# Kernel optimization log

Measured on AMD Instinct MI355X. Metric: run time of the kernel, lower is better.

Reference implementation:

```python
import jax, jax.numpy as jnp
import numpy as np

BETA = 0.01
EPS = 1e-6

def conv3x3(x, w, b):
    y = jax.lax.conv_general_dilated(x, w, (1, 1), 'SAME',
                                     dimension_numbers=('NCHW', 'OIHW', 'NCHW'))
    return y + b[None, :, None, None]

def variance_depth_flow(gt, patch, max_depth):
    B, C, H, W = gt.shape
    py, px = H // patch, W // patch
    # [B,C,py,px,P,P]
    p = gt.reshape(B, C, py, patch, px, patch).transpose(0, 1, 2, 4, 3, 5)
    p = jnp.where((p > 0.1) & (p < max_depth), p, jnp.zeros_like(p))
    bn = jnp.log(p[..., 0, :] + EPS)   # north border  [B,C,py,px,P]
    bs = jnp.log(p[..., -1, :] + EPS)  # south
    bw = jnp.log(p[..., :, 0] + EPS)   # west
    be = jnp.log(p[..., :, -1] + EPS)  # east
    def sx(b):  # shift patches left along x (axis=3), zero-pad last column
        return jnp.concatenate([b[:, :, :, 1:], jnp.zeros_like(b[:, :, :, :1])], axis=3)
    def sy(b):  # shift patches up along y (axis=2), zero-pad last row
        return jnp.concatenate([b[:, :, 1:], jnp.zeros_like(b[:, :, :1])], axis=2)
    diffs = [be - sx(bw), bs - sy(bn), be - sx(be), bs - sy(bs), bw - sx(bw),
             bn - sy(bn), bs - sx(bs), be - sy(be), bn - sx(bn), bw - sy(bw)]
    d = jnp.stack([x.sum(-1) for x in diffs], axis=-1)  # [B,C,py,px,10]
    d = d[:, 0].transpose(0, 3, 1, 2) / patch            # [B,10,py,px]
    return d

def smooth_l1(pred, target, beta):
    d = pred - target
    ad = jnp.abs(d)
    return jnp.where(ad < beta, 0.5 * d * d / beta, ad - 0.5 * beta)

def setup_inputs() -> dict:
    key = jax.random.key(0)
    ks = jax.random.split(key, 7)
    B, FC, DC, hw, HW = 32, 256, 64, 64, 512
    feat = jax.random.normal(ks[0], (B, FC, hw, hw), dtype=jnp.float32)
    depth = jax.random.normal(ks[1], (B, DC, hw, hw), dtype=jnp.float32)
    gts = jax.random.uniform(ks[2], (B, 1, HW, HW), dtype=jnp.float32)
    W_att = jax.random.normal(ks[3], (DC, FC, 3, 3), dtype=jnp.float32) * 0.02
    b_att = jnp.zeros((DC,), dtype=jnp.float32)
    W_post = jax.random.normal(ks[4], (10, DC, 3, 3), dtype=jnp.float32) * 0.05
    b_post = jnp.zeros((10,), dtype=jnp.float32)
    return {"feat": feat, "depth": depth, "gts": gts,
            "W_att": W_att, "b_att": b_att, "W_post": W_post, "b_post": b_post}

def reference(feat, depth, gts, W_att, b_att, W_post, b_post):
    max_depth = 80.0
    n, c, h, w = depth.shape
    patch = gts.shape[2] // h
    flow_gradient = variance_depth_flow(gts, patch, max_depth)  # [B,10,h,w]
    att = jax.nn.sigmoid(conv3x3(feat, W_att, b_att))           # [B,DC,h,w]
    ds = conv3x3(att * depth, W_post, b_post)                   # [B,10,h,w]
    diff = smooth_l1(ds, flow_gradient, BETA)
    return diff.sum() / (h * w * ds.shape[0] * ds.shape[1])
```

## Files before the change

kernel.cpp:

```cpp
#include <hip/hip_runtime.h>
#include <hip/hip_bf16.h>


typedef __attribute__((ext_vector_type(4))) float f32x4;
typedef __attribute__((ext_vector_type(8))) short s16x8;
typedef __attribute__((ext_vector_type(4))) unsigned int u32x4;

#define DEVFN __device__ __forceinline__

DEVFN float bf2f(unsigned short u){
  unsigned int x = ((unsigned int)u) << 16;
  float f; __builtin_memcpy(&f, &x, 4); return f;
}
DEVFN unsigned short f2bf(float f){
  unsigned int x; __builtin_memcpy(&x, &f, 4);
  x += 0x7fffu + ((x >> 16) & 1u);
  return (unsigned short)(x >> 16);
}
DEVFN unsigned cvtpk(float lo, float hi){
  unsigned r;
  asm("v_cvt_pk_bf16_f32 %0, %1, %2" : "=v"(r) : "v"(lo), "v"(hi));
  return r;
}

#define ASYNC16(gp, lp) __builtin_amdgcn_global_load_lds( \
    (const __attribute__((address_space(1))) unsigned int*)(gp), \
    (__attribute__((address_space(3))) unsigned int*)(lp), 16, 0, 0)

__global__ void k_weights(const float* __restrict__ Watt, const float* __restrict__ Wpost,
                          unsigned short* __restrict__ WT1, unsigned short* __restrict__ WT2){
  const int t = blockIdx.x * 256 + threadIdx.x;
  const int n1 = 9 * 64 * 256;
  if (t < n1){
    const int tap = t / (64 * 256);
    const int rem = t % (64 * 256);
    const int oc = rem / 256, ic = rem % 256;
    WT1[t] = f2bf(Watt[(oc * 256 + ic) * 9 + tap]);
  }
  const int n2 = 9 * 16 * 64;
  if (t < n2){
    const int tap = t / (16 * 64);
    const int rem = t % (16 * 64);
    const int od = rem / 64, ic = rem % 64;
    const float v = (od < 10) ? Wpost[(od * 64 + ic) * 9 + tap] : 0.0f;
    WT2[t] = f2bf(v);
  }
}

__global__ void k_borders(const float* __restrict__ gts, float* __restrict__ S,
                          float* __restrict__ out){
  const int bid = blockIdx.x, tid = threadIdx.x;
  if (bid == 0 && tid == 0) *out = 0.0f;
  __shared__ float slab[4096];
  const int rel = bid;
  const float* gp = gts + (size_t)rel * 4096;
#pragma unroll
  for (int it = 0; it < 4; ++it){
    const int id = it * 256 + tid;
    *(f32x4*)&slab[id * 4] = *(const f32x4*)&gp[id * 4];
  }
  __syncthreads();
  const int px = tid & 63, border = tid >> 6;
  float s = 0.0f;
#pragma unroll
  for (int i = 0; i < 8; ++i){
    float v;
    if (border == 0)      v = slab[px * 8 + i];
    else if (border == 1) v = slab[7 * 512 + px * 8 + i];
    else if (border == 2) v = slab[i * 512 + px * 8];
    else                  v = slab[i * 512 + px * 8 + 7];
    v = ((v > 0.1f) && (v < 80.0f)) ? v : 0.0f;
    s += __logf(v + 1e-6f);
  }
  S[((size_t)rel * 64 + px) * 4 + border] = s;
}

__global__ __launch_bounds__(256, 2) void k_gemm1(
    const float* __restrict__ feat,
    const unsigned short* __restrict__ WT1,
    const float* __restrict__ batt,
    const float* __restrict__ depth,
    unsigned short* __restrict__ adT)
{
  __shared__ unsigned short As[4 * 17 * 16 * 8];
  __shared__ unsigned short Bs[576 * 32];
  const int t = threadIdx.x;
  const int l = t & 63, wid = t >> 6;
  const int wm = wid & 1, wo = wid >> 1;
  const int b = blockIdx.x >> 5, ytile = blockIdx.x & 31;
  const int y0 = ytile * 2;
  const int fr = l & 15, g = l >> 4;

  f32x4 acc[4][2];
#pragma unroll
  for (int i = 0; i < 4; ++i)
#pragma unroll
    for (int j = 0; j < 2; ++j)
#pragma unroll
      for (int q = 0; q < 4; ++q) acc[i][j][q] = 0.0f;

  if (t < 64){
    const int yy = t >> 4, u = t & 15;
    u32x4 z = {0, 0, 0, 0};
    *(u32x4*)&As[((yy * 17 + 16) * 16 + u) * 8] = z;
  }

  f32x4 hold[8];
  auto loadRow = [&](int c){
    const int yr = y0 - 1 + wid;
    if (yr >= 0 && yr < 64){
      const float* gp = feat + ((size_t)(b * 256 + c * 32 + g * 8)) * 4096
                             + (size_t)yr * 64 + fr * 4;
#pragma unroll
      for (int e = 0; e < 8; ++e) hold[e] = *(const f32x4*)(gp + (size_t)e * 4096);
    } else {
#pragma unroll
      for (int e = 0; e < 8; ++e) hold[e] = f32x4{0.f, 0.f, 0.f, 0.f};
    }
  };
  auto cvtWriteRow = [&](){
#pragma unroll
    for (int o = 0; o < 4; ++o){
      u32x4 pk;
      pk[0] = cvtpk(hold[0][o], hold[1][o]);
      pk[1] = cvtpk(hold[2][o], hold[3][o]);
      pk[2] = cvtpk(hold[4][o], hold[5][o]);
      pk[3] = cvtpk(hold[6][o], hold[7][o]);
      const int u = 4 * ((g ^ fr) & 3) + ((o ^ (fr >> 1)) & 3);
      *(u32x4*)&As[((wid * 17 + fr) * 16 + u) * 8] = pk;
    }
  };
  auto stageB = [&](int c){
#pragma unroll
    for (int it = 0; it < 9; ++it){
      const int idx = it * 256 + t;
      const int row = idx >> 2;
      const int sg = (idx & 3) ^ ((row >> 1) & 3);
      ASYNC16(WT1 + (size_t)row * 256 + c * 32 + sg * 8, &Bs[(size_t)idx * 8]);
    }
  };
  auto compute = [&](){
    const int slotB = (g ^ ((fr >> 1) & 3)) * 8;
#pragma unroll
    for (int tap = 0; tap < 9; ++tap){
      const int dy = tap / 3 - 1, dx = tap % 3 - 1;
      const int yy = wm + dy + 1;
      const int rowb = yy * 17 * 16;
      s16x8 af[4], bfr[2];
#pragma unroll
      for (int i = 0; i < 4; ++i){
        const int x = i * 16 + fr + dx;
        const bool valid = (x >= 0) && (x < 64);
        const int xq = valid ? (x >> 2) : 16;
        const int u = valid ? (4 * ((g ^ (x >> 2)) & 3) + (((x & 3) ^ (x >> 3)) & 3))
                            : 4 * g;
        af[i] = *(const s16x8*)&As[(rowb + xq * 16 + u) * 8];
      }
#pragma unroll
      for (int j = 0; j < 2; ++j)
        bfr[j] = *(const s16x8*)&Bs[(tap * 64 + wo * 32 + j * 16 + fr) * 32 + slotB];
#pragma unroll
      for (int i = 0; i < 4; ++i)
#pragma unroll
        for (int j = 0; j < 2; ++j)
          acc[i][j] = __builtin_amdgcn_mfma_f32_16x16x32_bf16(af[i], bfr[j], acc[i][j], 0, 0, 0);
    }
  };

  loadRow(0);
  stageB(0);
  cvtWriteRow();
  __syncthreads();

  for (int c = 0; c < 8; ++c){
    if (c < 7) loadRow(c + 1);
    compute();
    __syncthreads();
    if (c < 7){
      cvtWriteRow();
      stageB(c + 1);
    }
    __syncthreads();
  }

  const int y = y0 + wm;
#pragma unroll
  for (int j = 0; j < 2; ++j){
    const int oc = wo * 32 + j * 16 + fr;
    const float bb = batt[oc];
    const float* dpt = depth + ((size_t)(b * 64 + oc)) * 4096 + (size_t)y * 64;
    unsigned short* op = adT + ((size_t)(b * 4096 + y * 64)) * 64 + oc;
#pragma unroll
    for (int i = 0; i < 4; ++i){
      const f32x4 dv4 = *(const f32x4*)&dpt[i * 16 + g * 4];
#pragma unroll
      for (int q = 0; q < 4; ++q){
        const int xo = i * 16 + g * 4 + q;
        const float v = acc[i][j][q] + bb;
        const float att = 1.0f / (1.0f + __expf(-v));
        op[(size_t)xo * 64] = f2bf(att * dv4[q]);
      }
    }
  }
}

DEVFN float sel4(f32x4 v, int i){
  const float ab = (i & 1) ? v[1] : v[0];
  const float cd = (i & 1) ? v[3] : v[2];
  return (i & 2) ? cd : ab;
}

__global__ __launch_bounds__(512, 2) void k_gemm2(
    const unsigned short* __restrict__ adT,
    const unsigned short* __restrict__ WT2,
    const float* __restrict__ bpost,
    const f32x4* __restrict__ S,
    float* __restrict__ out)
{
  __shared__ unsigned short As[2][20480];
  __shared__ unsigned short Bs[9216];
  __shared__ float ps[8];
  const int t = threadIdx.x;
  const int l = t & 63, w = t >> 6;
  const int b = blockIdx.x >> 3, ytile = blockIdx.x & 7;
  const int y0 = ytile * 8;
  const int fr = l & 15, g = l >> 4;

  f32x4 acc[4];
#pragma unroll
  for (int i = 0; i < 4; ++i)
#pragma unroll
    for (int q = 0; q < 4; ++q) acc[i][q] = 0.0f;

  auto stageA = [&](int c, int d){
#pragma unroll
    for (int it2 = 0; it2 < 5; ++it2){
      const int it = it2 * 2 + (t >> 8);
      const int yy = y0 - 1 + it;
      const int xx = (t >> 2) & 63, icg = t & 3;
      unsigned short* lp = &As[d][(it * 64 + xx) * 32 + icg * 8];
      if (yy >= 0 && yy < 64){
        const int sg = icg ^ ((xx >> 1) & 3);
        const unsigned short* gp = adT
            + ((size_t)(b * 4096 + yy * 64 + xx)) * 64 + c * 32 + sg * 8;
        ASYNC16(gp, lp);
      } else {
        s16x8 z = {0,0,0,0,0,0,0,0};
        *(s16x8*)lp = z;
      }
    }
  };
#pragma unroll
  for (int it = 0; it < 3; ++it){
    const int idx = it * 512 + t;
    if (idx < 1152){
      const int row = idx >> 3, p = idx & 7;
      const int sg = p ^ (row & 7);
      ASYNC16(WT2 + (size_t)row * 64 + sg * 8, Bs + (size_t)idx * 8);
    }
  }
  stageA(0, 0);
  __syncthreads();

  for (int c = 0; c < 2; ++c){
    if (c == 0) stageA(1, 1);
    const unsigned short* Ab = As[c];
    const int pB = ((c * 4 + g) ^ (fr & 7)) * 8;
    for (int tap = 0; tap < 9; ++tap){
      const int dy = tap / 3 - 1, dx = tap % 3 - 1;
      s16x8 af[4];
#pragma unroll
      for (int i = 0; i < 4; ++i){
        const int xv = i * 16 + fr + dx;
        const bool valid = (xv >= 0) && (xv < 64);
        const int xw = valid ? xv : 0;
        const int slot = (g ^ ((xw >> 1) & 3)) * 8;
        s16x8 v = *(const s16x8*)&Ab[((w + dy + 1) * 64 + xw) * 32 + slot];
        s16x8 z = {0,0,0,0,0,0,0,0};
        af[i] = valid ? v : z;
      }
      const s16x8 bfr = *(const s16x8*)&Bs[(tap * 16 + fr) * 64 + pB];
#pragma unroll
      for (int i = 0; i < 4; ++i)
        acc[i] = __builtin_amdgcn_mfma_f32_16x16x32_bf16(af[i], bfr, acc[i], 0, 0, 0);
    }
    __syncthreads();
  }

  const unsigned aPack = (3u<<0)|(1u<<2)|(3u<<4)|(1u<<6)|(2u<<8)|(0u<<10)|(1u<<12)|(3u<<14)|(0u<<16)|(2u<<18);
  const unsigned bPack = (2u<<0)|(0u<<2)|(3u<<4)|(1u<<6)|(2u<<8)|(0u<<10)|(1u<<12)|(3u<<14)|(0u<<16)|(2u<<18);
  float lsum = 0.0f;
  const int y = y0 + w;
  if (fr < 10){
    const int od = fr;
    const int ai = (aPack >> (2 * od)) & 3;
    const int bi = (bPack >> (2 * od)) & 3;
    const bool xshift = (od & 1) == 0;
    const float bp = bpost[od];
#pragma unroll
    for (int i = 0; i < 4; ++i){
#pragma unroll
      for (int q = 0; q < 4; ++q){
        const int xo = i * 16 + g * 4 + q;
        const size_t gm = (size_t)b * 4096 + (size_t)y * 64 + xo;
        const f32x4 sa = S[gm];
        const bool nb = xshift ? (xo < 63) : (y < 63);
        const size_t ga = xshift ? (nb ? gm + 1 : gm) : (nb ? gm + 64 : gm);
        const f32x4 sbv = S[ga];
        const float sbf = nb ? sel4(sbv, bi) : 0.0f;
        const float flow = (sel4(sa, ai) - sbf) * 0.125f;
        const float dv = acc[i][q] + bp - flow;
        const float adv = fabsf(dv);
        lsum += (adv < 0.01f) ? (50.0f * dv * dv) : (adv - 0.005f);
      }
    }
  }
#pragma unroll
  for (int off = 32; off > 0; off >>= 1) lsum += __shfl_down(lsum, off);
  if (l == 0) ps[w] = lsum;
  __syncthreads();
  if (t == 0){
    float s = 0.0f;
#pragma unroll
    for (int i = 0; i < 8; ++i) s += ps[i];
    atomicAdd(out, s * (1.0f / 1310720.0f));
  }
}

extern "C" void kernel_launch(void* const* d_in, const int* in_sizes, int n_in,
                              void* d_out, int out_size, void* d_ws, size_t ws_size,
                              hipStream_t stream){
  const float* feat  = (const float*)d_in[0];
  const float* depth = (const float*)d_in[1];
  const float* gts   = (const float*)d_in[2];
  const float* Watt  = (const float*)d_in[3];
  const float* batt  = (const float*)d_in[4];
  const float* Wpost = (const float*)d_in[5];
  const float* bpost = (const float*)d_in[6];
  float* out = (float*)d_out;
  char* ws = (char*)d_ws;

  unsigned short* adT = (unsigned short*)ws;
  unsigned short* WT1 = (unsigned short*)(ws + 16777216);
  unsigned short* WT2 = (unsigned short*)(ws + 16777216 + 294912);
  float*          S   = (float*)(ws + 16777216 + 294912 + 18432);

  k_weights<<<576, 256, 0, stream>>>(Watt, Wpost, WT1, WT2);
  k_gemm1<<<1024, 256, 0, stream>>>(feat, WT1, batt, depth, adT);
  k_borders<<<2048, 256, 0, stream>>>(gts, S, out);
  k_gemm2<<<256, 512, 0, stream>>>(adT, WT2, bpost, (const f32x4*)S, out);
}
```

Before: 94.07 us.

## Merge prep kernels and enlarge gemm1 tiles to four output rows per block

Fuses the weight-conversion and gts border-sum kernels into a single launch, removing one kernel launch. Reshapes conv1 so each 512-thread block computes four output rows instead of two, which improves reuse of the halo rows and staged weights. It also remaps block IDs across batches, simplifies the LDS swizzle, raises wave priority around the MFMA loop and issues the weight async loads before the activation writes. The risks are higher register and LDS pressure per block and two idle waves during row loads.

```diff
diff --git a/kernel.cpp b/kernel.cpp
--- a/kernel.cpp
+++ b/kernel.cpp
@@ -27,32 +27,33 @@
     (const __attribute__((address_space(1))) unsigned int*)(gp), \
     (__attribute__((address_space(3))) unsigned int*)(lp), 16, 0, 0)
 
-__global__ void k_weights(const float* __restrict__ Watt, const float* __restrict__ Wpost,
-                          unsigned short* __restrict__ WT1, unsigned short* __restrict__ WT2){
-  const int t = blockIdx.x * 256 + threadIdx.x;
-  const int n1 = 9 * 64 * 256;
-  if (t < n1){
-    const int tap = t / (64 * 256);
-    const int rem = t % (64 * 256);
-    const int oc = rem / 256, ic = rem % 256;
-    WT1[t] = f2bf(Watt[(oc * 256 + ic) * 9 + tap]);
-  }
-  const int n2 = 9 * 16 * 64;
-  if (t < n2){
-    const int tap = t / (16 * 64);
-    const int rem = t % (16 * 64);
-    const int od = rem / 64, ic = rem % 64;
-    const float v = (od < 10) ? Wpost[(od * 64 + ic) * 9 + tap] : 0.0f;
-    WT2[t] = f2bf(v);
-  }
-}
-
-__global__ void k_borders(const float* __restrict__ gts, float* __restrict__ S,
-                          float* __restrict__ out){
+__global__ void k_prep(const float* __restrict__ Watt, const float* __restrict__ Wpost,
+                       const float* __restrict__ gts,
+                       unsigned short* __restrict__ WT1, unsigned short* __restrict__ WT2,
+                       float* __restrict__ S, float* __restrict__ out){
   const int bid = blockIdx.x, tid = threadIdx.x;
   if (bid == 0 && tid == 0) *out = 0.0f;
+  if (bid < 576){
+    const int t = bid * 256 + tid;
+    const int n1 = 9 * 64 * 256;
+    if (t < n1){
+      const int tap = t / (64 * 256);
+      const int rem = t % (64 * 256);
+      const int oc = rem / 256, ic = rem % 256;
+      WT1[t] = f2bf(Watt[(oc * 256 + ic) * 9 + tap]);
+    }
+    const int n2 = 9 * 16 * 64;
+    if (t < n2){
+      const int tap = t / (16 * 64);
+      const int rem = t % (16 * 64);
+      const int od = rem / 64, ic = rem % 64;
+      const float v = (od < 10) ? Wpost[(od * 64 + ic) * 9 + tap] : 0.0f;
+      WT2[t] = f2bf(v);
+    }
+    return;
+  }
   __shared__ float slab[4096];
-  const int rel = bid;
+  const int rel = bid - 576;
   const float* gp = gts + (size_t)rel * 4096;
 #pragma unroll
   for (int it = 0; it < 4; ++it){
@@ -75,20 +76,21 @@
   S[((size_t)rel * 64 + px) * 4 + border] = s;
 }
 
-__global__ __launch_bounds__(256, 2) void k_gemm1(
+__global__ __launch_bounds__(512, 4) void k_gemm1(
     const float* __restrict__ feat,
     const unsigned short* __restrict__ WT1,
     const float* __restrict__ batt,
     const float* __restrict__ depth,
     unsigned short* __restrict__ adT)
 {
-  __shared__ unsigned short As[4 * 17 * 16 * 8];
+  __shared__ unsigned short As[6 * 17 * 16 * 8];
   __shared__ unsigned short Bs[576 * 32];
   const int t = threadIdx.x;
   const int l = t & 63, wid = t >> 6;
-  const int wm = wid & 1, wo = wid >> 1;
-  const int b = blockIdx.x >> 5, ytile = blockIdx.x & 31;
-  const int y0 = ytile * 2;
+  const int wm = wid & 3, wo = wid >> 2;
+  const int bid = (blockIdx.x & 7) * 64 + (blockIdx.x >> 3);
+  const int b = bid >> 4, ytile = bid & 15;
+  const int y0 = ytile * 4;
   const int fr = l & 15, g = l >> 4;
 
   f32x4 acc[4][2];
@@ -99,14 +101,15 @@
 #pragma unroll
       for (int q = 0; q < 4; ++q) acc[i][j][q] = 0.0f;
 
-  if (t < 64){
-    const int yy = t >> 4, u = t & 15;
+  if (t < 96){
+    const int yy = t >> 4, sp = t & 15;
     u32x4 z = {0, 0, 0, 0};
-    *(u32x4*)&As[((yy * 17 + 16) * 16 + u) * 8] = z;
+    *(u32x4*)&As[((yy * 17 + 16) * 16 + sp) * 8] = z;
   }
 
   f32x4 hold[8];
   auto loadRow = [&](int c){
+    if (wid >= 6) return;
     const int yr = y0 - 1 + wid;
     if (yr >= 0 && yr < 64){
       const float* gp = feat + ((size_t)(b * 256 + c * 32 + g * 8)) * 4096
@@ -119,6 +122,7 @@
     }
   };
   auto cvtWriteRow = [&](){
+    if (wid >= 6) return;
 #pragma unroll
     for (int o = 0; o < 4; ++o){
       u32x4 pk;
@@ -126,21 +130,24 @@
       pk[1] = cvtpk(hold[2][o], hold[3][o]);
       pk[2] = cvtpk(hold[4][o], hold[5][o]);
       pk[3] = cvtpk(hold[6][o], hold[7][o]);
-      const int u = 4 * ((g ^ fr) & 3) + ((o ^ (fr >> 1)) & 3);
-      *(u32x4*)&As[((wid * 17 + fr) * 16 + u) * 8] = pk;
+      const int sp = (4 * g + o) ^ fr;
+      *(u32x4*)&As[((wid * 17 + fr) * 16 + sp) * 8] = pk;
     }
   };
   auto stageB = [&](int c){
 #pragma unroll
-    for (int it = 0; it < 9; ++it){
-      const int idx = it * 256 + t;
-      const int row = idx >> 2;
-      const int sg = (idx & 3) ^ ((row >> 1) & 3);
-      ASYNC16(WT1 + (size_t)row * 256 + c * 32 + sg * 8, &Bs[(size_t)idx * 8]);
+    for (int it = 0; it < 5; ++it){
+      const int idx = it * 512 + t;
+      if (idx < 2304){
+        const int row = idx >> 2;
+        const int sg = (idx & 3) ^ ((row >> 1) & 3);
+        ASYNC16(WT1 + (size_t)row * 256 + c * 32 + sg * 8, &Bs[(size_t)idx * 8]);
+      }
     }
   };
   auto compute = [&](){
     const int slotB = (g ^ ((fr >> 1) & 3)) * 8;
+    __builtin_amdgcn_s_setprio(1);
 #pragma unroll
     for (int tap = 0; tap < 9; ++tap){
       const int dy = tap / 3 - 1, dx = tap % 3 - 1;
@@ -152,9 +159,8 @@
         const int x = i * 16 + fr + dx;
         const bool valid = (x >= 0) && (x < 64);
         const int xq = valid ? (x >> 2) : 16;
-        const int u = valid ? (4 * ((g ^ (x >> 2)) & 3) + (((x & 3) ^ (x >> 3)) & 3))
-                            : 4 * g;
-        af[i] = *(const s16x8*)&As[(rowb + xq * 16 + u) * 8];
+        const int sp = valid ? ((4 * g + (x & 3)) ^ (x >> 2)) : 4 * g;
+        af[i] = *(const s16x8*)&As[(rowb + xq * 16 + sp) * 8];
       }
 #pragma unroll
       for (int j = 0; j < 2; ++j)
@@ -165,6 +171,7 @@
         for (int j = 0; j < 2; ++j)
           acc[i][j] = __builtin_amdgcn_mfma_f32_16x16x32_bf16(af[i], bfr[j], acc[i][j], 0, 0, 0);
     }
+    __builtin_amdgcn_s_setprio(0);
   };
 
   loadRow(0);
@@ -177,8 +184,8 @@
     compute();
     __syncthreads();
     if (c < 7){
+      stageB(c + 1);
       cvtWriteRow();
-      stageB(c + 1);
     }
     __syncthreads();
   }
@@ -345,8 +352,7 @@
   unsigned short* WT2 = (unsigned short*)(ws + 16777216 + 294912);
   float*          S   = (float*)(ws + 16777216 + 294912 + 18432);
 
-  k_weights<<<576, 256, 0, stream>>>(Watt, Wpost, WT1, WT2);
-  k_gemm1<<<1024, 256, 0, stream>>>(feat, WT1, batt, depth, adT);
-  k_borders<<<2048, 256, 0, stream>>>(gts, S, out);
+  k_prep<<<576 + 2048, 256, 0, stream>>>(Watt, Wpost, gts, WT1, WT2, S, out);
+  k_gemm1<<<512, 512, 0, stream>>>(feat, WT1, batt, depth, adT);
   k_gemm2<<<256, 512, 0, stream>>>(adT, WT2, bpost, (const f32x4*)S, out);
 }
```

Result: faster. 89.47 us (-4.9%).
